# Kernel tuning notes

Hardware: AMD Instinct MI355X
Metric: run time of the kernel (lower is better)

The kernel has to match this reference:

```python
import jax, jax.numpy as jnp
import numpy as np

N_HEADS = 12
R = 0.5            # cfg.r kernel bandwidth
MASK_NEG = 10000.0


def _split_heads(t, n_heads):
    # (B, S, D) -> (B, H, S, W)
    B, S, D = t.shape
    return t.reshape(B, S, n_heads, D // n_heads).transpose(0, 2, 1, 3)


def setup_inputs() -> dict:
    key = jax.random.key(0)
    ks = jax.random.split(key, 8)
    B, S, D = 2, 256, 768
    sd = 1.0 / np.sqrt(D)
    x = jax.random.normal(ks[0], (B, S, D), dtype=jnp.float32)
    mask = jnp.ones((B, S), dtype=jnp.float32)
    Wq = jax.random.normal(ks[1], (D, D), dtype=jnp.float32) * sd
    bq = jnp.zeros((D,), dtype=jnp.float32)
    Wk = jax.random.normal(ks[2], (D, D), dtype=jnp.float32) * sd
    bk = jnp.zeros((D,), dtype=jnp.float32)
    Wv = jax.random.normal(ks[3], (D, D), dtype=jnp.float32) * sd
    bv = jnp.zeros((D,), dtype=jnp.float32)
    return {"x": x, "mask": mask, "Wq": Wq, "bq": bq, "Wk": Wk, "bk": bk, "Wv": Wv, "bv": bv}


def reference(x, mask, Wq, bq, Wk, bk, Wv, bv):
    B, S, D = x.shape
    H = N_HEADS
    # torch nn.Linear: y = x @ W.T + b
    q = _split_heads(x @ Wq.T + bq, H)   # (B, H, S, W)
    k = _split_heads(x @ Wk.T + bk, H)
    v = _split_heads(x @ Wv.T + bv, H)
    # sinc^4 product kernel over head width W: scores[b,h,l,i] = prod_w sinc(r*(q-k))^4
    diff = q[:, :, :, None, :] - k[:, :, None, :, :]          # (B, H, S, S, W)
    scores = jnp.prod(jnp.sinc(R * diff) ** 4, axis=-1)       # (B, H, S, S)
    scores = scores - MASK_NEG * (1.0 - mask[:, None, None, :])
    w = jax.nn.softmax(scores, axis=-1)                        # (B, H, S, S)
    y = w @ v                                                  # (B, H, S, W)
    y = y / w.sum(axis=-1, keepdims=True)                      # faithful (sums to 1)
    # merge heads: (B, H, S, W) -> (B, S, D)
    h = y.transpose(0, 2, 1, 3).reshape(B, S, D)
    return h
```

## Files before the change

### kernel.cpp

```cpp
#include <hip/hip_runtime.h>
#include <math.h>

#define NB 2
#define SS 256
#define DD 768
#define NH 12
#define WW 64

using f32x4  = __attribute__((ext_vector_type(4))) float;
using bf16x8 = __attribute__((ext_vector_type(8))) short;

constexpr float R2  = 0.25f;
constexpr float C8  = 4.1168160e-7f;
constexpr float EPS = 1e-4f;

#define QKV_ELEMS (NB*NH*SS*WW)
#define A_OFF_BYTES  4718592u
#define B_OFF_BYTES  6291456u
#define QT_OFF_BYTES 13369344u
#define KT_OFF_BYTES 18087936u

#define XBLKS 384
#define WBLKS 1728

__device__ __forceinline__ unsigned short bf16_rn(float f) {
    unsigned u = __builtin_bit_cast(unsigned, f);
    u += 0x7fffu + ((u >> 16) & 1u);
    return (unsigned short)(u >> 16);
}

__global__ __launch_bounds__(256) void conv_all(
        const float* __restrict__ x,
        const float* __restrict__ Wq, const float* __restrict__ Wk, const float* __restrict__ Wv,
        unsigned short* __restrict__ A, unsigned short* __restrict__ B) {
    int bid = blockIdx.x;
    const float* src;
    unsigned short* dstrow;
    if (bid < XBLKS) {
        int idx = bid * 256 + threadIdx.x;
        int m = idx / (DD/4);
        int c = (idx - m*(DD/4)) * 4;
        src = x + (size_t)idx * 4;
        dstrow = A + (size_t)m * 1536 + c;
    } else {
        int idx = (bid - XBLKS) * 256 + threadIdx.x;
        int p = idx / (768*192);
        int rem = idx - p*(768*192);
        const float* W = (p == 0) ? Wq : (p == 1) ? Wk : Wv;
        int j = rem / 192;
        int c = (rem - j*192) * 4;
        src = W + (size_t)rem * 4;
        dstrow = B + (size_t)(p*768 + j) * 1536 + c;
    }
    float4 v = *reinterpret_cast<const float4*>(src);
    float vv[4] = {v.x, v.y, v.z, v.w};
    unsigned short h[4], l[4];
    #pragma unroll
    for (int e = 0; e < 4; ++e) {
        h[e] = bf16_rn(vv[e]);
        float hf = __builtin_bit_cast(float, (unsigned)h[e] << 16);
        l[e] = bf16_rn(vv[e] - hf);
    }
    *reinterpret_cast<ushort4*>(dstrow)       = make_ushort4(h[0], h[1], h[2], h[3]);
    *reinterpret_cast<ushort4*>(dstrow + 768) = make_ushort4(l[0], l[1], l[2], l[3]);
}

__global__ __launch_bounds__(256, 2) void gemm_qkv(
        const unsigned short* __restrict__ A, const unsigned short* __restrict__ B,
        const float* __restrict__ bq, const float* __restrict__ bk, const float* __restrict__ bv,
        float* __restrict__ qkv) {
    __shared__ float red[4][32*32];
    const int tid = threadIdx.x;
    const int wid = tid >> 6, l = tid & 63;
    const int lr = l & 15, lo_ = l >> 4;
    const int m0 = blockIdx.x * 32, n0 = blockIdx.y * 32;

    const unsigned short* Ap = A + (size_t)(m0 + lr) * 1536 + wid * 192 + lo_ * 8;
    const unsigned short* Bp = B + (size_t)(n0 + lr) * 1536 + wid * 192 + lo_ * 8;

    f32x4 acc00 = 0.f, acc01 = 0.f, acc10 = 0.f, acc11 = 0.f;

    bf16x8 ca0, ca1, cb0, cb1, na0, na1, nb0, nb1;
    ca0 = *reinterpret_cast<const bf16x8*>(Ap);
    ca1 = *reinterpret_cast<const bf16x8*>(Ap + 16*1536);
    cb0 = *reinterpret_cast<const bf16x8*>(Bp);
    cb1 = *reinterpret_cast<const bf16x8*>(Bp + 16*1536);

    #pragma unroll
    for (int it = 0; it < 18; ++it) {
        if (it < 17) {
            const int it1 = it + 1;
            const int seg1 = it1 / 6, kk1 = it1 - seg1 * 6;
            const int ao = ((seg1 == 2) ? 768 : 0) + kk1 * 32;
            const int bo = ((seg1 == 1) ? 768 : 0) + kk1 * 32;
            na0 = *reinterpret_cast<const bf16x8*>(Ap + ao);
            na1 = *reinterpret_cast<const bf16x8*>(Ap + 16*1536 + ao);
            nb0 = *reinterpret_cast<const bf16x8*>(Bp + bo);
            nb1 = *reinterpret_cast<const bf16x8*>(Bp + 16*1536 + bo);
        }
        acc00 = __builtin_amdgcn_mfma_f32_16x16x32_bf16(ca0, cb0, acc00, 0, 0, 0);
        acc01 = __builtin_amdgcn_mfma_f32_16x16x32_bf16(ca0, cb1, acc01, 0, 0, 0);
        acc10 = __builtin_amdgcn_mfma_f32_16x16x32_bf16(ca1, cb0, acc10, 0, 0, 0);
        acc11 = __builtin_amdgcn_mfma_f32_16x16x32_bf16(ca1, cb1, acc11, 0, 0, 0);
        ca0 = na0; ca1 = na1; cb0 = nb0; cb1 = nb1;
    }

    #pragma unroll
    for (int j = 0; j < 4; ++j) {
        int r0 = lo_ * 4 + j;
        red[wid][(r0     ) * 32 + lr     ] = acc00[j];
        red[wid][(r0     ) * 32 + lr + 16] = acc01[j];
        red[wid][(r0 + 16) * 32 + lr     ] = acc10[j];
        red[wid][(r0 + 16) * 32 + lr + 16] = acc11[j];
    }
    __syncthreads();

    int row = tid >> 3, col = (tid & 7) * 4;
    f32x4 s = *reinterpret_cast<f32x4*>(&red[0][row*32 + col]);
    #pragma unroll
    for (int w = 1; w < 4; ++w)
        s += *reinterpret_cast<f32x4*>(&red[w][row*32 + col]);

    int n = n0 + col;
    int which = n / 768;
    int jj = n - which * 768;
    const float* bias = (which == 0) ? bq : (which == 1) ? bk : bv;
    float4 bb = *reinterpret_cast<const float4*>(&bias[jj]);
    s[0] += bb.x; s[1] += bb.y; s[2] += bb.z; s[3] += bb.w;

    int m = m0 + row, b_ = m >> 8, s_ = m & 255;
    int head = jj >> 6, w = jj & 63;
    float* o = qkv + (size_t)which * QKV_ELEMS + (((size_t)b_ * NH + head) * SS + s_) * WW + w;
    *reinterpret_cast<float4*>(o) = make_float4(s[0], s[1], s[2], s[3]);
}

__global__ __launch_bounds__(256) void prep(const float* __restrict__ qkv,
                                            float* __restrict__ QT, float* __restrict__ KT) {
    const int c = blockIdx.x, bh = blockIdx.y;
    const int lane = threadIdx.x & 63, wv = threadIdx.x >> 6;
    const int key = c * 64 + lane;
    const int d0 = wv * 16;
    const float* q = qkv + ((size_t)bh * SS + key) * WW + d0;
    const float* k = qkv + QKV_ELEMS + ((size_t)bh * SS + key) * WW + d0;
    float* qt = QT + ((size_t)bh * SS + key) * 3 * WW;
    float* kt = KT + (size_t)bh * WW * 3 * SS;
    #pragma unroll
    for (int g = 0; g < 4; ++g) {
        float4 qv = *reinterpret_cast<const float4*>(q + g * 4);
        float4 kv = *reinterpret_cast<const float4*>(k + g * 4);
        float qa[4] = {qv.x, qv.y, qv.z, qv.w};
        float ka[4] = {kv.x, kv.y, kv.z, kv.w};
        f32x4 qr, qs, qc;
        #pragma unroll
        for (int e = 0; e < 4; ++e) {
            float a = R2 * qa[e];
            qr[e] = a;
            qs[e] = __builtin_amdgcn_sinf(a);
            qc[e] = __builtin_amdgcn_cosf(a);
        }
        *reinterpret_cast<f32x4*>(qt + 0 * WW + d0 + g * 4) = qr;
        *reinterpret_cast<f32x4*>(qt + 1 * WW + d0 + g * 4) = qs;
        *reinterpret_cast<f32x4*>(qt + 2 * WW + d0 + g * 4) = qc;
        #pragma unroll
        for (int e = 0; e < 4; ++e) {
            float a = R2 * ka[e];
            int d = d0 + g * 4 + e;
            kt[(d * 3 + 0) * SS + key] = a;
            kt[(d * 3 + 1) * SS + key] = __builtin_amdgcn_sinf(a);
            kt[(d * 3 + 2) * SS + key] = __builtin_amdgcn_cosf(a);
        }
    }
}

__global__ __launch_bounds__(256, 3) void fattn(
    const float* __restrict__ qkv, const float* __restrict__ QT, const float* __restrict__ KT,
    const float* __restrict__ mask, float* __restrict__ out)
{
    const int bh = blockIdx.y;
    const int b = bh / NH, h = bh - b * NH;
    const int row0 = blockIdx.x * 8;

    const float* Vg = qkv + (size_t)(2 * QKV_ELEMS) + (size_t)bh * SS * WW;
    const float* kt = KT + (size_t)bh * WW * 3 * SS;

    __shared__ __align__(16) float qt[8][3][WW];
    __shared__ __align__(16) float ebuf[SS][8];
    __shared__ __align__(16) float ypart[4][8][WW];
    __shared__ float zs[4][8];

    const int tid = threadIdx.x, lane = tid & 63, wid = tid >> 6;

    {
        const f32x4* qsrc = reinterpret_cast<const f32x4*>(QT + ((size_t)bh * SS + row0) * 3 * WW);
        f32x4* qdst = reinterpret_cast<f32x4*>(&qt[0][0][0]);
        qdst[tid] = qsrc[tid];
        if (tid < 128) qdst[tid + 256] = qsrc[tid + 256];
    }
    const float mt = -10000.0f * (1.0f - mask[b * SS + tid]);
    __syncthreads();

    float pg[8] = {1.f,1.f,1.f,1.f,1.f,1.f,1.f,1.f};

    auto score_group = [&](int g) {
        const float* kg = kt + (size_t)g * 8 * 3 * SS + tid;
        float kk[8], sk[8], ck[8];
        #pragma unroll
        for (int j = 0; j < 8; ++j) {
            kk[j] = kg[j * 3 * SS];
            sk[j] = kg[j * 3 * SS + SS];
            ck[j] = kg[j * 3 * SS + 2 * SS];
        }
        #pragma unroll
        for (int r = 0; r < 8; ++r) {
            f32x4 q0 = *reinterpret_cast<const f32x4*>(&qt[r][0][g*8]);
            f32x4 q1 = *reinterpret_cast<const f32x4*>(&qt[r][0][g*8+4]);
            f32x4 s0 = *reinterpret_cast<const f32x4*>(&qt[r][1][g*8]);
            f32x4 s1 = *reinterpret_cast<const f32x4*>(&qt[r][1][g*8+4]);
            f32x4 c0 = *reinterpret_cast<const f32x4*>(&qt[r][2][g*8]);
            f32x4 c1 = *reinterpret_cast<const f32x4*>(&qt[r][2][g*8+4]);
            float ps = 1.f, pt = 1.f;
            #pragma unroll
            for (int j = 0; j < 8; ++j) {
                float qv = (j < 4) ? q0[j] : q1[j-4];
                float sq = (j < 4) ? s0[j] : s1[j-4];
                float cq = (j < 4) ? c0[j] : c1[j-4];
                float t  = qv - kk[j];
                float at = fmaxf(fabsf(t), EPS);
                float sn = fmaf(sq, ck[j], -(cq * sk[j]));
                sn = (fabsf(t) < EPS) ? at : sn;
                ps *= sn;
                pt *= at;
            }
            pg[r] *= (ps * C8) * __builtin_amdgcn_rcpf(pt);
        }
    };

    for (int g = 0; g < 3; ++g) score_group(g);

    float mx = fabsf(pg[0]);
    #pragma unroll
    for (int r = 1; r < 8; ++r) mx = fmaxf(mx, fabsf(pg[r]));
    if (__any(mx > 0.0078125f)) {
        for (int g = 3; g < 8; ++g) score_group(g);
    }

    float e[8];
    #pragma unroll
    for (int r = 0; r < 8; ++r) {
        float p = pg[r];
        p *= p; p *= p;
        e[r] = __expf(p + mt);
    }
    {
        f32x4 e0, e1;
        #pragma unroll
        for (int r = 0; r < 4; ++r) { e0[r] = e[r]; e1[r] = e[r+4]; }
        *reinterpret_cast<f32x4*>(&ebuf[tid][0]) = e0;
        *reinterpret_cast<f32x4*>(&ebuf[tid][4]) = e1;
    }
    #pragma unroll
    for (int r = 0; r < 8; ++r) {
        float z = e[r];
        #pragma unroll
        for (int off = 32; off; off >>= 1) z += __shfl_xor(z, off);
        if (lane == 0) zs[wid][r] = z;
    }

    float y[8] = {0.f,0.f,0.f,0.f,0.f,0.f,0.f,0.f};
    const float* vb = Vg + (size_t)(wid * 64) * WW + lane;
    #pragma unroll 16
    for (int ii = 0; ii < 64; ++ii) {
        float v = vb[ii * WW];
        f32x4 ea = *reinterpret_cast<const f32x4*>(&ebuf[wid*64 + ii][0]);
        f32x4 eb = *reinterpret_cast<const f32x4*>(&ebuf[wid*64 + ii][4]);
        y[0] = fmaf(ea[0], v, y[0]); y[1] = fmaf(ea[1], v, y[1]);
        y[2] = fmaf(ea[2], v, y[2]); y[3] = fmaf(ea[3], v, y[3]);
        y[4] = fmaf(eb[0], v, y[4]); y[5] = fmaf(eb[1], v, y[5]);
        y[6] = fmaf(eb[2], v, y[6]); y[7] = fmaf(eb[3], v, y[7]);
    }
    #pragma unroll
    for (int r = 0; r < 8; ++r) ypart[wid][r][lane] = y[r];
    __syncthreads();

    {
        const int r0 = tid >> 6;
        #pragma unroll
        for (int q = 0; q < 2; ++q) {
            int rr = r0 + q * 4;
            float yy = ypart[0][rr][lane] + ypart[1][rr][lane]
                     + ypart[2][rr][lane] + ypart[3][rr][lane];
            float zz = zs[0][rr] + zs[1][rr] + zs[2][rr] + zs[3][rr];
            out[((size_t)b * SS + row0 + rr) * DD + h * WW + lane] = yy * __builtin_amdgcn_rcpf(zz);
        }
    }
}

extern "C" void kernel_launch(void* const* d_in, const int* in_sizes, int n_in,
                              void* d_out, int out_size, void* d_ws, size_t ws_size,
                              hipStream_t stream) {
    const float* x    = (const float*)d_in[0];
    const float* mask = (const float*)d_in[1];
    const float* Wq   = (const float*)d_in[2];
    const float* bq   = (const float*)d_in[3];
    const float* Wk   = (const float*)d_in[4];
    const float* bk   = (const float*)d_in[5];
    const float* Wv   = (const float*)d_in[6];
    const float* bv   = (const float*)d_in[7];
    float* out = (float*)d_out;

    float*          qkv = (float*)d_ws;
    unsigned short* Ab  = (unsigned short*)((char*)d_ws + A_OFF_BYTES);
    unsigned short* Bb  = (unsigned short*)((char*)d_ws + B_OFF_BYTES);
    float*          QTp = (float*)((char*)d_ws + QT_OFF_BYTES);
    float*          KTp = (float*)((char*)d_ws + KT_OFF_BYTES);

    conv_all<<<dim3(XBLKS + WBLKS), 256, 0, stream>>>(x, Wq, Wk, Wv, Ab, Bb);
    gemm_qkv<<<dim3(512/32, 2304/32), 256, 0, stream>>>(Ab, Bb, bq, bk, bv, qkv);
    prep<<<dim3(4, NB*NH), 256, 0, stream>>>(qkv, QTp, KTp);
    fattn<<<dim3(SS/8, NB*NH), 256, 0, stream>>>(qkv, QTp, KTp, mask, out);
}
```

Before: 69.17 us.

## Fuse sin/cos prep into QKV GEMM epilogue and add per-row early exit

Removes the separate prep kernel by computing the scaled Q/K values and their sin/cos directly in the GEMM epilogue, writing QT/KT layouts there. This saves one launch and a round-trip of Q/K through global memory. The attention kernel's tail score loop now tracks liveness per query row and skips rows whose partial product is already below the threshold, breaking out once all rows are dead. The per-row checks add wave votes and branching, and the K stores from the GEMM epilogue are strided.

```diff
diff --git a/kernel.cpp b/kernel.cpp
--- a/kernel.cpp
+++ b/kernel.cpp
@@ -13,6 +13,7 @@
 constexpr float R2  = 0.25f;
 constexpr float C8  = 4.1168160e-7f;
 constexpr float EPS = 1e-4f;
+constexpr float THR = 0.0078125f;
 
 #define QKV_ELEMS (NB*NH*SS*WW)
 #define A_OFF_BYTES  4718592u
@@ -68,7 +69,7 @@
 __global__ __launch_bounds__(256, 2) void gemm_qkv(
         const unsigned short* __restrict__ A, const unsigned short* __restrict__ B,
         const float* __restrict__ bq, const float* __restrict__ bk, const float* __restrict__ bv,
-        float* __restrict__ qkv) {
+        float* __restrict__ qkv, float* __restrict__ QT, float* __restrict__ KT) {
     __shared__ float red[4][32*32];
     const int tid = threadIdx.x;
     const int wid = tid >> 6, l = tid & 63;
@@ -130,44 +131,33 @@
 
     int m = m0 + row, b_ = m >> 8, s_ = m & 255;
     int head = jj >> 6, w = jj & 63;
-    float* o = qkv + (size_t)which * QKV_ELEMS + (((size_t)b_ * NH + head) * SS + s_) * WW + w;
-    *reinterpret_cast<float4*>(o) = make_float4(s[0], s[1], s[2], s[3]);
-}
-
-__global__ __launch_bounds__(256) void prep(const float* __restrict__ qkv,
-                                            float* __restrict__ QT, float* __restrict__ KT) {
-    const int c = blockIdx.x, bh = blockIdx.y;
-    const int lane = threadIdx.x & 63, wv = threadIdx.x >> 6;
-    const int key = c * 64 + lane;
-    const int d0 = wv * 16;
-    const float* q = qkv + ((size_t)bh * SS + key) * WW + d0;
-    const float* k = qkv + QKV_ELEMS + ((size_t)bh * SS + key) * WW + d0;
-    float* qt = QT + ((size_t)bh * SS + key) * 3 * WW;
-    float* kt = KT + (size_t)bh * WW * 3 * SS;
-    #pragma unroll
-    for (int g = 0; g < 4; ++g) {
-        float4 qv = *reinterpret_cast<const float4*>(q + g * 4);
-        float4 kv = *reinterpret_cast<const float4*>(k + g * 4);
-        float qa[4] = {qv.x, qv.y, qv.z, qv.w};
-        float ka[4] = {kv.x, kv.y, kv.z, kv.w};
-        f32x4 qr, qs, qc;
+    int bh = b_ * NH + head;
+
+    if (which == 2) {
+        float* o = qkv + (size_t)2 * QKV_ELEMS + ((size_t)bh * SS + s_) * WW + w;
+        *reinterpret_cast<float4*>(o) = make_float4(s[0], s[1], s[2], s[3]);
+    } else if (which == 0) {
+        float* qtb = QT + ((size_t)bh * SS + s_) * 192 + w;
+        f32x4 av, sv, cv;
         #pragma unroll
         for (int e = 0; e < 4; ++e) {
-            float a = R2 * qa[e];
-            qr[e] = a;
-            qs[e] = __builtin_amdgcn_sinf(a);
-            qc[e] = __builtin_amdgcn_cosf(a);
-        }
-        *reinterpret_cast<f32x4*>(qt + 0 * WW + d0 + g * 4) = qr;
-        *reinterpret_cast<f32x4*>(qt + 1 * WW + d0 + g * 4) = qs;
-        *reinterpret_cast<f32x4*>(qt + 2 * WW + d0 + g * 4) = qc;
+            float a = R2 * s[e];
+            av[e] = a;
+            sv[e] = __builtin_amdgcn_sinf(a);
+            cv[e] = __builtin_amdgcn_cosf(a);
+        }
+        *reinterpret_cast<f32x4*>(qtb)       = av;
+        *reinterpret_cast<f32x4*>(qtb + 64)  = sv;
+        *reinterpret_cast<f32x4*>(qtb + 128) = cv;
+    } else {
+        float* ktb = KT + (size_t)bh * WW * 3 * SS;
         #pragma unroll
         for (int e = 0; e < 4; ++e) {
-            float a = R2 * ka[e];
-            int d = d0 + g * 4 + e;
-            kt[(d * 3 + 0) * SS + key] = a;
-            kt[(d * 3 + 1) * SS + key] = __builtin_amdgcn_sinf(a);
-            kt[(d * 3 + 2) * SS + key] = __builtin_amdgcn_cosf(a);
+            int d = w + e;
+            float a = R2 * s[e];
+            ktb[(d*3 + 0) * SS + s_] = a;
+            ktb[(d*3 + 1) * SS + s_] = __builtin_amdgcn_sinf(a);
+            ktb[(d*3 + 2) * SS + s_] = __builtin_amdgcn_cosf(a);
         }
     }
 }
@@ -237,11 +227,54 @@
 
     for (int g = 0; g < 3; ++g) score_group(g);
 
-    float mx = fabsf(pg[0]);
-    #pragma unroll
-    for (int r = 1; r < 8; ++r) mx = fmaxf(mx, fabsf(pg[r]));
-    if (__any(mx > 0.0078125f)) {
-        for (int g = 3; g < 8; ++g) score_group(g);
+    bool alive[8];
+    bool any8 = false;
+    #pragma unroll
+    for (int r = 0; r < 8; ++r) {
+        alive[r] = __any(fabsf(pg[r]) > THR);
+        any8 = any8 || alive[r];
+    }
+    if (any8) {
+        #pragma unroll 1
+        for (int g = 3; g < 8; ++g) {
+            const float* kg = kt + (size_t)g * 8 * 3 * SS + tid;
+            float kk[8], sk[8], ck[8];
+            #pragma unroll
+            for (int j = 0; j < 8; ++j) {
+                kk[j] = kg[j * 3 * SS];
+                sk[j] = kg[j * 3 * SS + SS];
+                ck[j] = kg[j * 3 * SS + 2 * SS];
+            }
+            bool still = false;
+            #pragma unroll
+            for (int r = 0; r < 8; ++r) {
+                if (alive[r]) {
+                    f32x4 q0 = *reinterpret_cast<const f32x4*>(&qt[r][0][g*8]);
+                    f32x4 q1 = *reinterpret_cast<const f32x4*>(&qt[r][0][g*8+4]);
+                    f32x4 s0 = *reinterpret_cast<const f32x4*>(&qt[r][1][g*8]);
+                    f32x4 s1 = *reinterpret_cast<const f32x4*>(&qt[r][1][g*8+4]);
+                    f32x4 c0 = *reinterpret_cast<const f32x4*>(&qt[r][2][g*8]);
+                    f32x4 c1 = *reinterpret_cast<const f32x4*>(&qt[r][2][g*8+4]);
+                    float ps = 1.f, pt = 1.f;
+                    #pragma unroll
+                    for (int j = 0; j < 8; ++j) {
+                        float qv = (j < 4) ? q0[j] : q1[j-4];
+                        float sq = (j < 4) ? s0[j] : s1[j-4];
+                        float cq = (j < 4) ? c0[j] : c1[j-4];
+                        float t  = qv - kk[j];
+                        float at = fmaxf(fabsf(t), EPS);
+                        float sn = fmaf(sq, ck[j], -(cq * sk[j]));
+                        sn = (fabsf(t) < EPS) ? at : sn;
+                        ps *= sn;
+                        pt *= at;
+                    }
+                    pg[r] *= (ps * C8) * __builtin_amdgcn_rcpf(pt);
+                    alive[r] = __any(fabsf(pg[r]) > THR);
+                }
+                still = still || alive[r];
+            }
+            if (!still) break;
+        }
     }
 
     float e[8];
@@ -315,7 +348,6 @@
     float*          KTp = (float*)((char*)d_ws + KT_OFF_BYTES);
 
     conv_all<<<dim3(XBLKS + WBLKS), 256, 0, stream>>>(x, Wq, Wk, Wv, Ab, Bb);
-    gemm_qkv<<<dim3(512/32, 2304/32), 256, 0, stream>>>(Ab, Bb, bq, bk, bv, qkv);
-    prep<<<dim3(4, NB*NH), 256, 0, stream>>>(qkv, QTp, KTp);
+    gemm_qkv<<<dim3(512/32, 2304/32), 256, 0, stream>>>(Ab, Bb, bq, bk, bv, qkv, QTp, KTp);
     fattn<<<dim3(SS/8, NB*NH), 256, 0, stream>>>(qkv, QTp, KTp, mask, out);
 }
```

Result: faster. 58.78 us (-15.0%).
